# Optimization experiments

Hardware: AMD Instinct MI355X
Metric: run time of the kernel (lower is better)

## Reference

```python
import jax, jax.numpy as jnp
import numpy as np
from jax import lax

K = 3      # kernel_size
PAD = 1    # padding
OG = 2     # offset groups


def _conv2d(x, w, b):
    y = lax.conv_general_dilated(x, w, (1, 1), [(PAD, PAD), (PAD, PAD)],
                                 dimension_numbers=('NCHW', 'OIHW', 'NCHW'))
    return y + b[None, :, None, None]


def _deform_conv2d(x, offset, mask, weight):
    # torchvision-style modulated deform_conv2d (v2), stride=1, dilation=1,
    # zero out-of-bounds, offset layout [B, OG*K*K*2, H, W] with (dy, dx) pairs.
    B, C, H, W = x.shape
    O = weight.shape[0]
    K2 = K * K
    Cg = C // OG

    ki, kj = jnp.meshgrid(jnp.arange(K), jnp.arange(K), indexing='ij')
    ki = ki.reshape(K2)
    kj = kj.reshape(K2)
    base_y = jnp.arange(H)[None, :] - PAD + ki[:, None]   # [K2, H]
    base_x = jnp.arange(W)[None, :] - PAD + kj[:, None]   # [K2, W]

    off = offset.reshape(B, OG, K2, 2, H, W)
    py = off[:, :, :, 0] + base_y[None, None, :, :, None].astype(x.dtype)  # [B,OG,K2,H,W]
    px = off[:, :, :, 1] + base_x[None, None, :, None, :].astype(x.dtype)
    m = mask.reshape(B, OG, K2, H, W)

    y0f = jnp.floor(py)
    x0f = jnp.floor(px)
    wy1 = py - y0f   # bilinear weights, grads flow through py/px
    wx1 = px - x0f
    y0 = y0f.astype(jnp.int32)
    x0 = x0f.astype(jnp.int32)
    y1 = y0 + 1
    x1 = x0 + 1

    img = x.reshape(B, OG, Cg, H * W)

    def gather(yi, xi):
        valid = (yi >= 0) & (yi < H) & (xi >= 0) & (xi < W)
        idx = jnp.clip(yi, 0, H - 1) * W + jnp.clip(xi, 0, W - 1)          # [B,OG,K2,H,W]
        v = jnp.take_along_axis(img[:, :, :, None, :],
                                idx.reshape(B, OG, 1, K2, H * W), axis=-1)
        return v.reshape(B, OG, Cg, K2, H, W) * valid[:, :, None].astype(x.dtype)

    v00 = gather(y0, x0)
    v01 = gather(y0, x1)
    v10 = gather(y1, x0)
    v11 = gather(y1, x1)

    wy1e = wy1[:, :, None]   # [B,OG,1,K2,H,W]
    wx1e = wx1[:, :, None]
    val = (v00 * (1 - wy1e) * (1 - wx1e)
           + v01 * (1 - wy1e) * wx1e
           + v10 * wy1e * (1 - wx1e)
           + v11 * wy1e * wx1e)
    val = val * m[:, :, None]                               # modulation mask

    wr = weight.reshape(O, OG, Cg, K2)
    return jnp.einsum('ogck,bgckhw->bohw', wr, val)


def setup_inputs() -> dict:
    key = jax.random.key(0)
    k1, k2, k3, k4, k5 = jax.random.split(key, 5)
    B, C, O, H, W = 4, 64, 64, 128, 128
    K2 = K * K
    x = jax.random.normal(k1, (B, C, H, W), dtype=jnp.float32)
    w_main = jax.random.normal(k2, (O, C, K, K), dtype=jnp.float32) / np.sqrt(C * K2)
    w_off = jax.random.normal(k3, (2 * OG * K2, C, K, K), dtype=jnp.float32) * 0.01
    b_off = jax.random.normal(k4, (2 * OG * K2,), dtype=jnp.float32) * 0.01
    w_mask = jnp.full((OG * K2, C, K, K), 0.5, dtype=jnp.float32)  # init_mask = 0.5
    b_mask = jax.random.normal(k5, (OG * K2,), dtype=jnp.float32) * 0.01
    return {"x": x, "w_main": w_main, "w_off": w_off, "b_off": b_off,
            "w_mask": w_mask, "b_mask": b_mask}


def reference(x, w_main, w_off, b_off, w_mask, b_mask):
    offset = _conv2d(x, w_off, b_off)
    mask = jax.nn.sigmoid(_conv2d(x, w_mask, b_mask))
    return _deform_conv2d(x, offset, mask, w_main)
```

## Files before the change

### kernel.cpp

```cpp
#include <hip/hip_runtime.h>
#include <math.h>

#define BB 4
#define C 64
#define O 64
#define H 128
#define W 128
#define K2 9
#define HW (H*W)
#define NOFF 36

typedef __bf16 bf16;
typedef bf16 bf16x8 __attribute__((ext_vector_type(8)));
typedef float f32x4 __attribute__((ext_vector_type(4)));
typedef unsigned short u16x8 __attribute__((ext_vector_type(8)));
typedef unsigned int u32x4 __attribute__((ext_vector_type(4)));

#define BSTR 55
#define VSTR 36
#define VAL_BYTES 12288
#define B2A_OFF 12288
#define B2B_OFF 14592
#define B2C_OFF 16896
#define SMEM_BYTES 19200
#define WFRAG 18432
#define NW_TOTAL 73728

__device__ inline unsigned short f2h_bits(float f) {
  _Float16 h = (_Float16)f;
  return __builtin_bit_cast(unsigned short, h);
}
__device__ inline float h2f(unsigned short u) {
  return (float)__builtin_bit_cast(_Float16, u);
}
__device__ inline int soff(int row, int chunk) {
  return row * 64 + ((chunk ^ (row & 7)) * 8);
}

__global__ __launch_bounds__(256) void prep_all(
    const float* __restrict__ x, const float* __restrict__ w_main,
    const float* __restrict__ w_off, const float* __restrict__ w_mask,
    unsigned short* __restrict__ xT16, bf16* __restrict__ wfC,
    bf16* __restrict__ wfM) {
  __shared__ float tile[64][69];
  int tid = threadIdx.x;
  int b = blockIdx.x >> 8;
  int p0 = (blockIdx.x & 255) * 64;
#pragma unroll
  for (int it = 0; it < 4; ++it) {
    int c = it * 16 + (tid >> 4);
    int p4 = (tid & 15) * 4;
    *(f32x4*)&tile[c][p4] =
        *(const f32x4*)(x + (size_t)(b * C + c) * HW + p0 + p4);
  }
  __syncthreads();
#pragma unroll
  for (int it = 0; it < 2; ++it) {
    int t = it * 256 + tid;
    int p = t >> 3;
    int h8 = t & 7;
    u16x8 o;
#pragma unroll
    for (int j = 0; j < 8; ++j) {
      bf16 v = (bf16)tile[h8 * 8 + j][p];
      o[j] = __builtin_bit_cast(unsigned short, v);
    }
    *(u16x8*)&xT16[(size_t)(b * HW + p0 + p) * C + h8 * 8] = o;
  }
  int i = blockIdx.x * 256 + tid;
  if (i < NW_TOTAL) {
    int which = (i >= 36864);
    int ii = which ? i - 36864 : i;
    int j = ii & 7;
    int l = (ii >> 3) & 63;
    int rest = ii >> 9;
    int to = rest & 3;
    int kk = (rest >> 2) % 9;
    int ph = (rest >> 2) / 9;
    int m = to * 16 + (l & 15);
    int u = kk * 32 + (l >> 4) * 8 + j;
    int tap = u >> 5;
    int c1 = u & 31;
    if (!which) {
      int c = ph * 32 + c1;
      float v = (m < NOFF) ? w_off[(m * C + c) * K2 + tap]
                : (m < 54) ? w_mask[((m - NOFF) * C + c) * K2 + tap]
                           : 0.f;
      wfC[ii] = (bf16)v;
    } else {
      wfM[ii] = (bf16)w_main[(m * C + ph * 32 + c1) * K2 + tap];
    }
  }
}

__global__ __launch_bounds__(256, 8) void fused_deform(
    const bf16* __restrict__ xT, const bf16* __restrict__ wfC,
    const bf16* __restrict__ wfM, const float* __restrict__ b_off,
    const float* __restrict__ b_mask, float* __restrict__ out) {
  __shared__ __align__(16) char smem[SMEM_BYTES];
  bf16* stage = (bf16*)smem;
  float* bufF = (float*)smem;
  float* valF = (float*)smem;
  bf16* val = (bf16*)smem;
  unsigned int* buf2a = (unsigned int*)(smem + B2A_OFF);
  unsigned int* buf2b = (unsigned int*)(smem + B2B_OFF);
  unsigned int* buf2c = (unsigned int*)(smem + B2C_OFF);

  const int tid = threadIdx.x;
  const int lane = tid & 63;
  const int wv = tid >> 6;
  const int n16 = lane & 15;
  const int q4 = lane >> 4;
  const int to = wv;
  const int pg = tid >> 3;
  const int ch = tid & 7;

  const int g8 = blockIdx.x & 7;
  const int slot = blockIdx.x >> 3;
  const int b = g8 >> 1;
  const int ti = (g8 & 1) * 256 + slot;
  const int h0 = ti >> 2;
  const int w0 = (ti & 3) * 32;
  const bf16* xb = xT + (size_t)b * HW * C;

  bf16x8 zero8;
#pragma unroll
  for (int j = 0; j < 8; ++j) zero8[j] = (bf16)0.f;

#pragma unroll
  for (int it = 0; it < 4; ++it) {
    int id = it * 256 + tid;
    if (id < 816) {
      int chk = id & 7;
      int rest = id >> 3;
      int wp = rest % 34;
      int r = rest / 34;
      int yy = h0 + r - 1;
      int xx = w0 + wp - 1;
      bf16x8 v = zero8;
      if ((unsigned)yy < (unsigned)H && (unsigned)xx < (unsigned)W)
        v = *(const bf16x8*)(xb + (size_t)((yy << 7) + xx) * C + chk * 8);
      *(bf16x8*)(stage + soff(r * 34 + wp, chk)) = v;
    }
  }
  __syncthreads();
  f32x4 accC[2] = {{0.f,0.f,0.f,0.f},{0.f,0.f,0.f,0.f}};
#pragma unroll 1
  for (int ph = 0; ph < 2; ++ph) {
#pragma unroll
    for (int kk = 0; kk < 9; ++kk) {
      bf16x8 afr = *(const bf16x8*)(wfC +
          (size_t)(((ph * 9 + kk) * 4 + to) * 64 + lane) * 8);
#pragma unroll
      for (int nt = 0; nt < 2; ++nt) {
        int row = (kk / 3) * 34 + nt * 16 + n16 + kk % 3;
        bf16x8 bfr = *(const bf16x8*)(stage + soff(row, ph * 4 + q4));
        accC[nt] = __builtin_amdgcn_mfma_f32_16x16x32_bf16(afr, bfr, accC[nt], 0, 0, 0);
      }
    }
  }
  __syncthreads();

#pragma unroll
  for (int nt = 0; nt < 2; ++nt)
#pragma unroll
    for (int r = 0; r < 4; ++r) {
      int o = to * 16 + q4 * 4 + r;
      int p = nt * 16 + n16;
      float a = accC[nt][r];
      if (o < NOFF) {
        bufF[p * BSTR + o] = a + b_off[o];
      } else if (o < 54) {
        float s = a + b_mask[o - NOFF];
        bufF[p * BSTR + o] = 1.f / (1.f + __expf(-s));
      }
    }
  __syncthreads();

#pragma unroll
  for (int it = 0; it < 3; ++it) {
    int t = it * 256 + tid;
    if (t < 576) {
      int p = t & 31;
      int gk = t >> 5;
      int tap = gk % 9;
      float offy = bufF[p * BSTR + 2 * gk];
      float offx = bufF[p * BSTR + 2 * gk + 1];
      float m = bufF[p * BSTR + NOFF + gk];
      float py = offy + (float)(h0 + tap / 3 - 1);
      float px = offx + (float)(w0 + p + tap % 3 - 1);
      float y0f = floorf(py), x0f = floorf(px);
      float wy1 = py - y0f, wx1 = px - x0f;
      float wy0 = 1.f - wy1, wx0 = 1.f - wx1;
      int y0 = (int)y0f, x0 = (int)x0f;
      int y1 = y0 + 1, x1 = x0 + 1;
      bool y0ok = (unsigned)y0 < (unsigned)H, y1ok = (unsigned)y1 < (unsigned)H;
      bool x0ok = (unsigned)x0 < (unsigned)W, x1ok = (unsigned)x1 < (unsigned)W;
      float w00 = (y0ok && x0ok) ? wy0 * wx0 * m : 0.f;
      float w01 = (y0ok && x1ok) ? wy0 * wx1 * m : 0.f;
      float w10 = (y1ok && x0ok) ? wy1 * wx0 * m : 0.f;
      float w11 = (y1ok && x1ok) ? wy1 * wx1 * m : 0.f;
      unsigned int y0c = (unsigned)min(max(y0, 0), H - 1);
      unsigned int y1c = (unsigned)min(max(y1, 0), H - 1);
      unsigned int x0c = (unsigned)min(max(x0, 0), W - 1);
      unsigned int x1c = (unsigned)min(max(x1, 0), W - 1);
      int idx = p * 18 + gk;
      buf2a[idx] = (unsigned)f2h_bits(w00) | ((unsigned)f2h_bits(w01) << 16);
      buf2b[idx] = (unsigned)f2h_bits(w10) | ((unsigned)f2h_bits(w11) << 16);
      buf2c[idx] = y0c | (x0c << 8) | (y1c << 16) | (x1c << 24);
    }
  }
  __syncthreads();

  f32x4 accM[2] = {{0.f,0.f,0.f,0.f},{0.f,0.f,0.f,0.f}};
  const bf16* bb = xb + ch * 8;
  const int gg = ch >> 2;
#pragma unroll 1
  for (int kc = 0; kc < 3; ++kc) {
    if (kc) __syncthreads();
#pragma unroll
    for (int t = 0; t < 3; ++t) {
      int tap = kc * 3 + t;
      int idx = pg * 18 + gg * 9 + tap;
      unsigned wA = buf2a[idx];
      unsigned wB = buf2b[idx];
      unsigned co = buf2c[idx];
      float w00 = h2f(wA & 0xffff), w01 = h2f(wA >> 16);
      float w10 = h2f(wB & 0xffff), w11 = h2f(wB >> 16);
      int r0 = (int)(co & 255) << 7;
      int x0 = (int)((co >> 8) & 255);
      int r1 = (int)((co >> 16) & 255) << 7;
      int x1 = (int)(co >> 24);
      bf16x8 v00 = *(const bf16x8*)(bb + (size_t)(r0 + x0) * C);
      bf16x8 v01 = *(const bf16x8*)(bb + (size_t)(r0 + x1) * C);
      bf16x8 v10 = *(const bf16x8*)(bb + (size_t)(r1 + x0) * C);
      bf16x8 v11 = *(const bf16x8*)(bb + (size_t)(r1 + x1) * C);
      bf16x8 res;
#pragma unroll
      for (int j = 0; j < 8; ++j) {
        float v = (float)v00[j] * w00 + (float)v01[j] * w01 +
                  (float)v10[j] * w10 + (float)v11[j] * w11;
        res[j] = (bf16)v;
      }
      *(bf16x8*)(val + soff(t * 32 + pg, ch)) = res;
    }
    __syncthreads();
#pragma unroll
    for (int t = 0; t < 3; ++t) {
      int tap = kc * 3 + t;
#pragma unroll
      for (int g = 0; g < 2; ++g) {
        bf16x8 afr = *(const bf16x8*)(wfM + (size_t)g * WFRAG +
            (size_t)((tap * 4 + to) * 64 + lane) * 8);
#pragma unroll
        for (int nt = 0; nt < 2; ++nt) {
          int row = t * 32 + nt * 16 + n16;
          bf16x8 bfr = *(const bf16x8*)(val + soff(row, g * 4 + q4));
          accM[nt] = __builtin_amdgcn_mfma_f32_16x16x32_bf16(afr, bfr, accM[nt], 0, 0, 0);
        }
      }
    }
  }

  __syncthreads();
#pragma unroll
  for (int nt = 0; nt < 2; ++nt)
#pragma unroll
    for (int r = 0; r < 4; ++r)
      valF[(to * 16 + q4 * 4 + r) * VSTR + nt * 16 + n16] = accM[nt][r];
  __syncthreads();
  {
    float* ob = out + (size_t)b * O * HW + (h0 << 7) + w0;
#pragma unroll
    for (int it = 0; it < 2; ++it) {
      int id = it * 256 + tid;
      int o = id >> 3, seg = id & 7;
      f32x4 v = *(f32x4*)&valF[o * VSTR + seg * 4];
      *(f32x4*)&ob[(size_t)o * HW + seg * 4] = v;
    }
  }
}

extern "C" void kernel_launch(void* const* d_in, const int* in_sizes, int n_in,
                              void* d_out, int out_size, void* d_ws,
                              size_t ws_size, hipStream_t stream) {
  const float* x = (const float*)d_in[0];
  const float* w_main = (const float*)d_in[1];
  const float* w_off = (const float*)d_in[2];
  const float* b_off = (const float*)d_in[3];
  const float* w_mask = (const float*)d_in[4];
  const float* b_mask = (const float*)d_in[5];
  float* out = (float*)d_out;

  unsigned short* xT16 = (unsigned short*)d_ws;
  bf16* wfC = (bf16*)(xT16 + (size_t)BB * HW * C);
  bf16* wfM = wfC + 36864;

  prep_all<<<1024, 256, 0, stream>>>(x, w_main, w_off, w_mask, xT16, wfC, wfM);
  fused_deform<<<2048, 256, 0, stream>>>((const bf16*)xT16, wfC, wfM, b_off,
                                         b_mask, out);
}
```

Measured before the change: 105.2 us.

## Build MFMA B fragments directly in registers from bilinear gathers, dropping LDS staging

Each wave now produces its MFMA B-operand fragments straight in registers from the bilinear sampling, so the interpolated values no longer go through a shared-memory staging buffer. This removes the per-chunk __syncthreads and the LDS write/read round trip. Waves are remapped so each one covers 16 pixels and 2 output tiles instead of 32 pixels and 1 output tile. The cost is that each wave recomputes the interpolation for its pixel subset, so every sample is computed twice across the pair of waves sharing pixels. The shared buffer offsets are also moved so the float output staging no longer overlaps the sampling tables, since the final store now comes without a preceding barrier.

```diff
diff --git a/kernel.cpp b/kernel.cpp
--- a/kernel.cpp
+++ b/kernel.cpp
@@ -18,11 +18,10 @@
 
 #define BSTR 55
 #define VSTR 36
-#define VAL_BYTES 12288
-#define B2A_OFF 12288
-#define B2B_OFF 14592
-#define B2C_OFF 16896
-#define SMEM_BYTES 19200
+#define B2A_OFF 13056
+#define B2B_OFF 15360
+#define B2C_OFF 17664
+#define SMEM_BYTES 19968
 #define WFRAG 18432
 #define NW_TOTAL 73728
 
@@ -101,7 +100,6 @@
   bf16* stage = (bf16*)smem;
   float* bufF = (float*)smem;
   float* valF = (float*)smem;
-  bf16* val = (bf16*)smem;
   unsigned int* buf2a = (unsigned int*)(smem + B2A_OFF);
   unsigned int* buf2b = (unsigned int*)(smem + B2B_OFF);
   unsigned int* buf2c = (unsigned int*)(smem + B2C_OFF);
@@ -112,8 +110,6 @@
   const int n16 = lane & 15;
   const int q4 = lane >> 4;
   const int to = wv;
-  const int pg = tid >> 3;
-  const int ch = tid & 7;
 
   const int g8 = blockIdx.x & 7;
   const int slot = blockIdx.x >> 3;
@@ -213,61 +209,71 @@
   __syncthreads();
 
   f32x4 accM[2] = {{0.f,0.f,0.f,0.f},{0.f,0.f,0.f,0.f}};
-  const bf16* bb = xb + ch * 8;
-  const int gg = ch >> 2;
+  const int ntm = wv & 1;
+  const int toh = wv >> 1;
+  const int px = ntm * 16 + n16;
+  const bf16* g0p = xb + q4 * 8;
+  const bf16* g1p = xb + 32 + q4 * 8;
 #pragma unroll 1
-  for (int kc = 0; kc < 3; ++kc) {
-    if (kc) __syncthreads();
-#pragma unroll
-    for (int t = 0; t < 3; ++t) {
-      int tap = kc * 3 + t;
-      int idx = pg * 18 + gg * 9 + tap;
-      unsigned wA = buf2a[idx];
-      unsigned wB = buf2b[idx];
-      unsigned co = buf2c[idx];
-      float w00 = h2f(wA & 0xffff), w01 = h2f(wA >> 16);
-      float w10 = h2f(wB & 0xffff), w11 = h2f(wB >> 16);
-      int r0 = (int)(co & 255) << 7;
-      int x0 = (int)((co >> 8) & 255);
-      int r1 = (int)((co >> 16) & 255) << 7;
-      int x1 = (int)(co >> 24);
-      bf16x8 v00 = *(const bf16x8*)(bb + (size_t)(r0 + x0) * C);
-      bf16x8 v01 = *(const bf16x8*)(bb + (size_t)(r0 + x1) * C);
-      bf16x8 v10 = *(const bf16x8*)(bb + (size_t)(r1 + x0) * C);
-      bf16x8 v11 = *(const bf16x8*)(bb + (size_t)(r1 + x1) * C);
-      bf16x8 res;
+  for (int tap = 0; tap < 9; ++tap) {
+    int i0 = px * 18 + tap;
+    int i1 = i0 + 9;
+    unsigned wA0 = buf2a[i0], wB0 = buf2b[i0], co0 = buf2c[i0];
+    unsigned wA1 = buf2a[i1], wB1 = buf2b[i1], co1 = buf2c[i1];
+    int ry0 = (int)(co0 & 255) << 7, rx0 = (int)((co0 >> 8) & 255);
+    int ry1 = (int)((co0 >> 16) & 255) << 7, rx1 = (int)(co0 >> 24);
+    int sy0 = (int)(co1 & 255) << 7, sx0 = (int)((co1 >> 8) & 255);
+    int sy1 = (int)((co1 >> 16) & 255) << 7, sx1 = (int)(co1 >> 24);
+    bf16x8 u00 = *(const bf16x8*)(g0p + (size_t)(ry0 + rx0) * C);
+    bf16x8 u01 = *(const bf16x8*)(g0p + (size_t)(ry0 + rx1) * C);
+    bf16x8 u10 = *(const bf16x8*)(g0p + (size_t)(ry1 + rx0) * C);
+    bf16x8 u11 = *(const bf16x8*)(g0p + (size_t)(ry1 + rx1) * C);
+    bf16x8 s00 = *(const bf16x8*)(g1p + (size_t)(sy0 + sx0) * C);
+    bf16x8 s01 = *(const bf16x8*)(g1p + (size_t)(sy0 + sx1) * C);
+    bf16x8 s10 = *(const bf16x8*)(g1p + (size_t)(sy1 + sx0) * C);
+    bf16x8 s11 = *(const bf16x8*)(g1p + (size_t)(sy1 + sx1) * C);
+    {
+      float w00 = h2f(wA0 & 0xffff), w01 = h2f(wA0 >> 16);
+      float w10 = h2f(wB0 & 0xffff), w11 = h2f(wB0 >> 16);
+      bf16x8 bfr;
 #pragma unroll
       for (int j = 0; j < 8; ++j) {
-        float v = (float)v00[j] * w00 + (float)v01[j] * w01 +
-                  (float)v10[j] * w10 + (float)v11[j] * w11;
-        res[j] = (bf16)v;
-      }
-      *(bf16x8*)(val + soff(t * 32 + pg, ch)) = res;
-    }
-    __syncthreads();
-#pragma unroll
-    for (int t = 0; t < 3; ++t) {
-      int tap = kc * 3 + t;
-#pragma unroll
-      for (int g = 0; g < 2; ++g) {
-        bf16x8 afr = *(const bf16x8*)(wfM + (size_t)g * WFRAG +
-            (size_t)((tap * 4 + to) * 64 + lane) * 8);
-#pragma unroll
-        for (int nt = 0; nt < 2; ++nt) {
-          int row = t * 32 + nt * 16 + n16;
-          bf16x8 bfr = *(const bf16x8*)(val + soff(row, g * 4 + q4));
-          accM[nt] = __builtin_amdgcn_mfma_f32_16x16x32_bf16(afr, bfr, accM[nt], 0, 0, 0);
-        }
-      }
-    }
-  }
-
-  __syncthreads();
-#pragma unroll
-  for (int nt = 0; nt < 2; ++nt)
+        float v = (float)u00[j] * w00 + (float)u01[j] * w01 +
+                  (float)u10[j] * w10 + (float)u11[j] * w11;
+        bfr[j] = (bf16)v;
+      }
+#pragma unroll
+      for (int i = 0; i < 2; ++i) {
+        bf16x8 afr = *(const bf16x8*)(wfM +
+            (size_t)((tap * 4 + 2 * toh + i) * 64 + lane) * 8);
+        accM[i] = __builtin_amdgcn_mfma_f32_16x16x32_bf16(afr, bfr, accM[i], 0, 0, 0);
+      }
+    }
+    {
+      float w00 = h2f(wA1 & 0xffff), w01 = h2f(wA1 >> 16);
+      float w10 = h2f(wB1 & 0xffff), w11 = h2f(wB1 >> 16);
+      bf16x8 bfr;
+#pragma unroll
+      for (int j = 0; j < 8; ++j) {
+        float v = (float)s00[j] * w00 + (float)s01[j] * w01 +
+                  (float)s10[j] * w10 + (float)s11[j] * w11;
+        bfr[j] = (bf16)v;
+      }
+#pragma unroll
+      for (int i = 0; i < 2; ++i) {
+        bf16x8 afr = *(const bf16x8*)(wfM + (size_t)WFRAG +
+            (size_t)((tap * 4 + 2 * toh + i) * 64 + lane) * 8);
+        accM[i] = __builtin_amdgcn_mfma_f32_16x16x32_bf16(afr, bfr, accM[i], 0, 0, 0);
+      }
+    }
+  }
+
+#pragma unroll
+  for (int i = 0; i < 2; ++i)
 #pragma unroll
     for (int r = 0; r < 4; ++r)
-      valF[(to * 16 + q4 * 4 + r) * VSTR + nt * 16 + n16] = accM[nt][r];
+      valF[((2 * toh + i) * 16 + q4 * 4 + r) * VSTR + ntm * 16 + n16] =
+          accM[i][r];
   __syncthreads();
   {
     float* ob = out + (size_t)b * O * HW + (h0 << 7) + w0;
```

Measured after the change: 157.6 us. 49.9% more time.

## Double-buffer deformable sampling tiles and overlap gather loads with MFMA

Applied to the files above, without the earlier changes.

Splits the val tile in shared memory into two buffers. The bilinear gather loads for the next tap chunk are issued before the current chunk's MFMA work, and the combine-and-store into the other buffer happens afterwards, leaving one barrier per chunk. This aims to hide global gather latency behind matrix math. In exchange, shared memory grows from about 19 KB to 31 KB, launch bounds drop occupancy from 8 to 5 blocks, and register pressure rises from holding 12 prefetched vectors.

```diff
diff --git a/kernel.cpp b/kernel.cpp
--- a/kernel.cpp
+++ b/kernel.cpp
@@ -18,11 +18,11 @@
 
 #define BSTR 55
 #define VSTR 36
-#define VAL_BYTES 12288
-#define B2A_OFF 12288
-#define B2B_OFF 14592
-#define B2C_OFF 16896
-#define SMEM_BYTES 19200
+#define VAL1_OFF 12288
+#define B2A_OFF 24576
+#define B2B_OFF 26880
+#define B2C_OFF 29184
+#define SMEM_BYTES 31488
 #define WFRAG 18432
 #define NW_TOTAL 73728
 
@@ -93,7 +93,7 @@
   }
 }
 
-__global__ __launch_bounds__(256, 8) void fused_deform(
+__global__ __launch_bounds__(256, 5) void fused_deform(
     const bf16* __restrict__ xT, const bf16* __restrict__ wfC,
     const bf16* __restrict__ wfM, const float* __restrict__ b_off,
     const float* __restrict__ b_mask, float* __restrict__ out) {
@@ -101,7 +101,8 @@
   bf16* stage = (bf16*)smem;
   float* bufF = (float*)smem;
   float* valF = (float*)smem;
-  bf16* val = (bf16*)smem;
+  bf16* val0 = (bf16*)smem;
+  bf16* val1 = (bf16*)(smem + VAL1_OFF);
   unsigned int* buf2a = (unsigned int*)(smem + B2A_OFF);
   unsigned int* buf2b = (unsigned int*)(smem + B2B_OFF);
   unsigned int* buf2c = (unsigned int*)(smem + B2C_OFF);
@@ -215,36 +216,53 @@
   f32x4 accM[2] = {{0.f,0.f,0.f,0.f},{0.f,0.f,0.f,0.f}};
   const bf16* bb = xb + ch * 8;
   const int gg = ch >> 2;
+
+#pragma unroll
+  for (int t = 0; t < 3; ++t) {
+    int idx = pg * 18 + gg * 9 + t;
+    unsigned wA = buf2a[idx], wB = buf2b[idx], co = buf2c[idx];
+    float w00 = h2f(wA & 0xffff), w01 = h2f(wA >> 16);
+    float w10 = h2f(wB & 0xffff), w11 = h2f(wB >> 16);
+    int r0 = (int)(co & 255) << 7;
+    int x0 = (int)((co >> 8) & 255);
+    int r1 = (int)((co >> 16) & 255) << 7;
+    int x1 = (int)(co >> 24);
+    bf16x8 v00 = *(const bf16x8*)(bb + (size_t)(r0 + x0) * C);
+    bf16x8 v01 = *(const bf16x8*)(bb + (size_t)(r0 + x1) * C);
+    bf16x8 v10 = *(const bf16x8*)(bb + (size_t)(r1 + x0) * C);
+    bf16x8 v11 = *(const bf16x8*)(bb + (size_t)(r1 + x1) * C);
+    bf16x8 res;
+#pragma unroll
+    for (int j = 0; j < 8; ++j) {
+      float v = (float)v00[j] * w00 + (float)v01[j] * w01 +
+                (float)v10[j] * w10 + (float)v11[j] * w11;
+      res[j] = (bf16)v;
+    }
+    *(bf16x8*)(val0 + soff(t * 32 + pg, ch)) = res;
+  }
+  __syncthreads();
+
 #pragma unroll 1
   for (int kc = 0; kc < 3; ++kc) {
-    if (kc) __syncthreads();
-#pragma unroll
-    for (int t = 0; t < 3; ++t) {
-      int tap = kc * 3 + t;
-      int idx = pg * 18 + gg * 9 + tap;
-      unsigned wA = buf2a[idx];
-      unsigned wB = buf2b[idx];
-      unsigned co = buf2c[idx];
-      float w00 = h2f(wA & 0xffff), w01 = h2f(wA >> 16);
-      float w10 = h2f(wB & 0xffff), w11 = h2f(wB >> 16);
-      int r0 = (int)(co & 255) << 7;
-      int x0 = (int)((co >> 8) & 255);
-      int r1 = (int)((co >> 16) & 255) << 7;
-      int x1 = (int)(co >> 24);
-      bf16x8 v00 = *(const bf16x8*)(bb + (size_t)(r0 + x0) * C);
-      bf16x8 v01 = *(const bf16x8*)(bb + (size_t)(r0 + x1) * C);
-      bf16x8 v10 = *(const bf16x8*)(bb + (size_t)(r1 + x0) * C);
-      bf16x8 v11 = *(const bf16x8*)(bb + (size_t)(r1 + x1) * C);
-      bf16x8 res;
-#pragma unroll
-      for (int j = 0; j < 8; ++j) {
-        float v = (float)v00[j] * w00 + (float)v01[j] * w01 +
-                  (float)v10[j] * w10 + (float)v11[j] * w11;
-        res[j] = (bf16)v;
-      }
-      *(bf16x8*)(val + soff(t * 32 + pg, ch)) = res;
-    }
-    __syncthreads();
+    const bf16* cur = (kc & 1) ? val1 : val0;
+    bf16* nxt = (kc & 1) ? val0 : val1;
+    bf16x8 hv[3][4];
+    if (kc < 2) {
+#pragma unroll
+      for (int t = 0; t < 3; ++t) {
+        unsigned co = buf2c[pg * 18 + gg * 9 + (kc + 1) * 3 + t];
+        int r0 = (int)(co & 255) << 7;
+        int x0 = (int)((co >> 8) & 255);
+        int r1 = (int)((co >> 16) & 255) << 7;
+        int x1 = (int)(co >> 24);
+        hv[t][0] = *(const bf16x8*)(bb + (size_t)(r0 + x0) * C);
+        hv[t][1] = *(const bf16x8*)(bb + (size_t)(r0 + x1) * C);
+        hv[t][2] = *(const bf16x8*)(bb + (size_t)(r1 + x0) * C);
+        hv[t][3] = *(const bf16x8*)(bb + (size_t)(r1 + x1) * C);
+      }
+    }
+    __builtin_amdgcn_sched_barrier(0);
+    __builtin_amdgcn_s_setprio(1);
 #pragma unroll
     for (int t = 0; t < 3; ++t) {
       int tap = kc * 3 + t;
@@ -255,14 +273,33 @@
 #pragma unroll
         for (int nt = 0; nt < 2; ++nt) {
           int row = t * 32 + nt * 16 + n16;
-          bf16x8 bfr = *(const bf16x8*)(val + soff(row, g * 4 + q4));
+          bf16x8 bfr = *(const bf16x8*)(cur + soff(row, g * 4 + q4));
           accM[nt] = __builtin_amdgcn_mfma_f32_16x16x32_bf16(afr, bfr, accM[nt], 0, 0, 0);
         }
       }
     }
-  }
-
-  __syncthreads();
+    __builtin_amdgcn_s_setprio(0);
+    __builtin_amdgcn_sched_barrier(0);
+    if (kc < 2) {
+#pragma unroll
+      for (int t = 0; t < 3; ++t) {
+        int idx = pg * 18 + gg * 9 + (kc + 1) * 3 + t;
+        unsigned wA = buf2a[idx], wB = buf2b[idx];
+        float w00 = h2f(wA & 0xffff), w01 = h2f(wA >> 16);
+        float w10 = h2f(wB & 0xffff), w11 = h2f(wB >> 16);
+        bf16x8 res;
+#pragma unroll
+        for (int j = 0; j < 8; ++j) {
+          float v = (float)hv[t][0][j] * w00 + (float)hv[t][1][j] * w01 +
+                    (float)hv[t][2][j] * w10 + (float)hv[t][3][j] * w11;
+          res[j] = (bf16)v;
+        }
+        *(bf16x8*)(nxt + soff(t * 32 + pg, ch)) = res;
+      }
+    }
+    __syncthreads();
+  }
+
 #pragma unroll
   for (int nt = 0; nt < 2; ++nt)
 #pragma unroll
```

Result: slower. 115.4 us (+9.7%).

## Split waves into bilinear-gather producers and MFMA consumers with LDS flag ring

Applied to the files above, without the earlier changes.

Replaces the barrier-separated phases (all four waves gather three taps, then all run MFMAs) with warp specialization. Two waves gather and interpolate one tap at a time into a three-slot LDS ring. The other two waves run the MFMA products for two output tiles each. The handoff uses volatile producer/consumer flags in shared memory, polled with s_sleep, instead of block-wide __syncthreads. The goal is to overlap gather latency with matrix work inside a block. The cost is that only half the waves issue the memory-heavy gathers, and the spin-polling adds overhead.

```diff
diff --git a/kernel.cpp b/kernel.cpp
--- a/kernel.cpp
+++ b/kernel.cpp
@@ -18,11 +18,12 @@
 
 #define BSTR 55
 #define VSTR 36
-#define VAL_BYTES 12288
+#define VAL_SLOT 2048
 #define B2A_OFF 12288
 #define B2B_OFF 14592
 #define B2C_OFF 16896
-#define SMEM_BYTES 19200
+#define FLG_OFF 19200
+#define SMEM_BYTES 19456
 #define WFRAG 18432
 #define NW_TOTAL 73728
 
@@ -105,6 +106,8 @@
   unsigned int* buf2a = (unsigned int*)(smem + B2A_OFF);
   unsigned int* buf2b = (unsigned int*)(smem + B2B_OFF);
   unsigned int* buf2c = (unsigned int*)(smem + B2C_OFF);
+  volatile unsigned int* prod = (volatile unsigned int*)(smem + FLG_OFF);
+  volatile unsigned int* cons = prod + 18;
 
   const int tid = threadIdx.x;
   const int lane = tid & 63;
@@ -112,16 +115,16 @@
   const int n16 = lane & 15;
   const int q4 = lane >> 4;
   const int to = wv;
-  const int pg = tid >> 3;
-  const int ch = tid & 7;
 
   const int g8 = blockIdx.x & 7;
-  const int slot = blockIdx.x >> 3;
+  const int slot0 = blockIdx.x >> 3;
   const int b = g8 >> 1;
-  const int ti = (g8 & 1) * 256 + slot;
+  const int ti = (g8 & 1) * 256 + slot0;
   const int h0 = ti >> 2;
   const int w0 = (ti & 3) * 32;
   const bf16* xb = xT + (size_t)b * HW * C;
+
+  if (tid < 36) prod[tid] = 0u;
 
   bf16x8 zero8;
 #pragma unroll
@@ -212,63 +215,99 @@
   }
   __syncthreads();
 
-  f32x4 accM[2] = {{0.f,0.f,0.f,0.f},{0.f,0.f,0.f,0.f}};
-  const bf16* bb = xb + ch * 8;
-  const int gg = ch >> 2;
+  if (wv < 2) {
+    const int pgp = tid >> 2;
+    const int ch2 = tid & 3;
+    const bf16* bb0 = xb + ch2 * 8;
+    const bf16* bb1 = xb + (ch2 + 4) * 8;
 #pragma unroll 1
-  for (int kc = 0; kc < 3; ++kc) {
-    if (kc) __syncthreads();
-#pragma unroll
-    for (int t = 0; t < 3; ++t) {
-      int tap = kc * 3 + t;
-      int idx = pg * 18 + gg * 9 + tap;
-      unsigned wA = buf2a[idx];
-      unsigned wB = buf2b[idx];
-      unsigned co = buf2c[idx];
-      float w00 = h2f(wA & 0xffff), w01 = h2f(wA >> 16);
-      float w10 = h2f(wB & 0xffff), w11 = h2f(wB >> 16);
-      int r0 = (int)(co & 255) << 7;
-      int x0 = (int)((co >> 8) & 255);
-      int r1 = (int)((co >> 16) & 255) << 7;
-      int x1 = (int)(co >> 24);
-      bf16x8 v00 = *(const bf16x8*)(bb + (size_t)(r0 + x0) * C);
-      bf16x8 v01 = *(const bf16x8*)(bb + (size_t)(r0 + x1) * C);
-      bf16x8 v10 = *(const bf16x8*)(bb + (size_t)(r1 + x0) * C);
-      bf16x8 v11 = *(const bf16x8*)(bb + (size_t)(r1 + x1) * C);
-      bf16x8 res;
-#pragma unroll
-      for (int j = 0; j < 8; ++j) {
-        float v = (float)v00[j] * w00 + (float)v01[j] * w01 +
-                  (float)v10[j] * w10 + (float)v11[j] * w11;
-        res[j] = (bf16)v;
-      }
-      *(bf16x8*)(val + soff(t * 32 + pg, ch)) = res;
-    }
-    __syncthreads();
-#pragma unroll
-    for (int t = 0; t < 3; ++t) {
-      int tap = kc * 3 + t;
+    for (int t = 0; t < 9; ++t) {
+      if (t >= 3) {
+        while (cons[2 * (t - 3)] == 0u || cons[2 * (t - 3) + 1] == 0u)
+          __builtin_amdgcn_s_sleep(1);
+      }
+      bf16* dst = val + (t % 3) * VAL_SLOT;
+      int i0 = pgp * 18 + t;
+      int i1 = i0 + 9;
+      unsigned co0 = buf2c[i0], co1 = buf2c[i1];
+      int r0 = (int)(co0 & 255) << 7, x0 = (int)((co0 >> 8) & 255);
+      int r1 = (int)((co0 >> 16) & 255) << 7, x1 = (int)(co0 >> 24);
+      int s0 = (int)(co1 & 255) << 7, z0 = (int)((co1 >> 8) & 255);
+      int s1 = (int)((co1 >> 16) & 255) << 7, z1 = (int)(co1 >> 24);
+      bf16x8 u00 = *(const bf16x8*)(bb0 + (size_t)(r0 + x0) * C);
+      bf16x8 u01 = *(const bf16x8*)(bb0 + (size_t)(r0 + x1) * C);
+      bf16x8 u10 = *(const bf16x8*)(bb0 + (size_t)(r1 + x0) * C);
+      bf16x8 u11 = *(const bf16x8*)(bb0 + (size_t)(r1 + x1) * C);
+      bf16x8 v00 = *(const bf16x8*)(bb1 + (size_t)(s0 + z0) * C);
+      bf16x8 v01 = *(const bf16x8*)(bb1 + (size_t)(s0 + z1) * C);
+      bf16x8 v10 = *(const bf16x8*)(bb1 + (size_t)(s1 + z0) * C);
+      bf16x8 v11 = *(const bf16x8*)(bb1 + (size_t)(s1 + z1) * C);
+      unsigned wA0 = buf2a[i0], wB0 = buf2b[i0];
+      unsigned wA1 = buf2a[i1], wB1 = buf2b[i1];
+      {
+        float a0 = h2f(wA0 & 0xffff), a1 = h2f(wA0 >> 16);
+        float a2 = h2f(wB0 & 0xffff), a3 = h2f(wB0 >> 16);
+        bf16x8 res;
+#pragma unroll
+        for (int j = 0; j < 8; ++j) {
+          float v = (float)u00[j] * a0 + (float)u01[j] * a1 +
+                    (float)u10[j] * a2 + (float)u11[j] * a3;
+          res[j] = (bf16)v;
+        }
+        *(bf16x8*)(dst + soff(pgp, ch2)) = res;
+      }
+      {
+        float a0 = h2f(wA1 & 0xffff), a1 = h2f(wA1 >> 16);
+        float a2 = h2f(wB1 & 0xffff), a3 = h2f(wB1 >> 16);
+        bf16x8 res;
+#pragma unroll
+        for (int j = 0; j < 8; ++j) {
+          float v = (float)v00[j] * a0 + (float)v01[j] * a1 +
+                    (float)v10[j] * a2 + (float)v11[j] * a3;
+          res[j] = (bf16)v;
+        }
+        *(bf16x8*)(dst + soff(pgp, ch2 + 4)) = res;
+      }
+      __threadfence_block();
+      if (lane == 0) prod[2 * t + wv] = 1u;
+    }
+  } else {
+    const int wv2 = wv - 2;
+    f32x4 acc[2][2] = {{{0.f,0.f,0.f,0.f},{0.f,0.f,0.f,0.f}},
+                       {{0.f,0.f,0.f,0.f},{0.f,0.f,0.f,0.f}}};
+#pragma unroll 1
+    for (int t = 0; t < 9; ++t) {
+      while (prod[2 * t] == 0u || prod[2 * t + 1] == 0u)
+        __builtin_amdgcn_s_sleep(1);
+      const bf16* src = val + (t % 3) * VAL_SLOT;
 #pragma unroll
       for (int g = 0; g < 2; ++g) {
-        bf16x8 afr = *(const bf16x8*)(wfM + (size_t)g * WFRAG +
-            (size_t)((tap * 4 + to) * 64 + lane) * 8);
-#pragma unroll
-        for (int nt = 0; nt < 2; ++nt) {
-          int row = t * 32 + nt * 16 + n16;
-          bf16x8 bfr = *(const bf16x8*)(val + soff(row, g * 4 + q4));
-          accM[nt] = __builtin_amdgcn_mfma_f32_16x16x32_bf16(afr, bfr, accM[nt], 0, 0, 0);
+        bf16x8 bfr0 = *(const bf16x8*)(src + soff(n16, g * 4 + q4));
+        bf16x8 bfr1 = *(const bf16x8*)(src + soff(16 + n16, g * 4 + q4));
+#pragma unroll
+        for (int i = 0; i < 2; ++i) {
+          int tox = wv2 * 2 + i;
+          bf16x8 afr = *(const bf16x8*)(wfM + (size_t)g * WFRAG +
+              (size_t)((t * 4 + tox) * 64 + lane) * 8);
+          acc[i][0] = __builtin_amdgcn_mfma_f32_16x16x32_bf16(afr, bfr0, acc[i][0], 0, 0, 0);
+          acc[i][1] = __builtin_amdgcn_mfma_f32_16x16x32_bf16(afr, bfr1, acc[i][1], 0, 0, 0);
         }
       }
-    }
-  }
-
-  __syncthreads();
-#pragma unroll
-  for (int nt = 0; nt < 2; ++nt)
-#pragma unroll
-    for (int r = 0; r < 4; ++r)
-      valF[(to * 16 + q4 * 4 + r) * VSTR + nt * 16 + n16] = accM[nt][r];
-  __syncthreads();
+      __threadfence_block();
+      if (lane == 0) cons[2 * t + wv2] = 1u;
+    }
+    while (cons[16] == 0u || cons[17] == 0u) __builtin_amdgcn_s_sleep(1);
+#pragma unroll
+    for (int i = 0; i < 2; ++i)
+#pragma unroll
+      for (int nt = 0; nt < 2; ++nt)
+#pragma unroll
+        for (int r = 0; r < 4; ++r)
+          valF[((wv2 * 2 + i) * 16 + q4 * 4 + r) * VSTR + nt * 16 + n16] =
+              acc[i][nt][r];
+  }
+  __syncthreads();
+
   {
     float* ob = out + (size_t)b * O * HW + (h0 << 7) + w0;
 #pragma unroll
```

After: 110.5 us. +5.1%, slower.
